# Optimization experiments

Measured on AMD Instinct MI355X. Metric: run time of the kernel, lower is better.

Reference implementation:

```python
import jax, jax.numpy as jnp
import numpy as np

NUM_CAMS, BS, NUM_QUERY, MAX_LEN, EMBED_DIMS, NPTS = 6, 1, 40000, 10000, 256, 4


def setup_inputs() -> dict:
    key = jax.random.key(0)
    kq, kr, km = jax.random.split(key, 3)
    query = jax.random.normal(kq, (BS, NUM_QUERY, EMBED_DIMS), dtype=jnp.float32)
    reference_points_cam = jax.random.normal(
        kr, (NUM_CAMS, BS, NUM_QUERY, NPTS, 2), dtype=jnp.float32)
    bev_mask = jax.random.randint(km, (NUM_CAMS, BS, NUM_QUERY, NPTS), 0, 2).astype(jnp.int32)
    return {"query": query, "reference_points_cam": reference_points_cam, "bev_mask": bev_mask}


def reference(query, reference_points_cam, bev_mask):
    # valid[c, q]: query q is seen by camera c (any of the NPTS mask bits set); bs == 1
    valid = (bev_mask > 0).any(-1)            # (cams, bs, Q) bool
    valid0 = valid[:, 0]                      # (cams, Q)

    # Stable stream compaction: valid indices first, in ascending query order.
    order = jnp.argsort(~valid0, axis=-1, stable=True)      # (cams, Q)
    indexes = order[:, :MAX_LEN].astype(jnp.int32)          # (cams, max_len)
    indexes_len = jnp.minimum(valid0.sum(-1), MAX_LEN).astype(jnp.int32)  # (cams,)

    # Padded gather/rebatch; zero out slots beyond each camera's valid count.
    pos_ok = jnp.arange(MAX_LEN)[None, :] < indexes_len[:, None]          # (cams, max_len)
    queries_rebatch = query[0][indexes]                                   # (cams, max_len, E)
    queries_rebatch = jnp.where(pos_ok[:, :, None], queries_rebatch, 0.0)

    ref0 = reference_points_cam[:, 0]                                     # (cams, Q, NPTS, 2)
    reference_points_rebatch = jax.vmap(lambda r, i: r[i])(ref0, indexes) # (cams, max_len, NPTS, 2)
    reference_points_rebatch = jnp.where(
        pos_ok[:, :, None, None], reference_points_rebatch, 0.0)

    # count_norm: 1 / (number of cameras that see each query, clamped to >= 1)
    count = valid.astype(jnp.float32).sum(0)                 # (bs, Q)
    count_norm = (1.0 / jnp.maximum(count, 1.0))[..., None]  # (bs, Q, 1)

    return (indexes,
            indexes_len,
            queries_rebatch.reshape(BS * NUM_CAMS, MAX_LEN, EMBED_DIMS),
            reference_points_rebatch.reshape(BS * NUM_CAMS, MAX_LEN, NPTS, 2),
            count_norm)
```

## Files before the change

kernel.cpp:

```cpp
#include <hip/hip_runtime.h>
#include <hip/hip_bf16.h>

#define NUM_CAMS 6
#define NQ       40000
#define MAX_LEN  10000
#define ED       256
#define NBLK     ((NQ + 255) / 256)

#define OFF_IDX  0
#define OFF_LEN  (NUM_CAMS * MAX_LEN)
#define OFF_Q    (OFF_LEN + NUM_CAMS)
#define OFF_REF  (OFF_Q + NUM_CAMS * MAX_LEN * ED)
#define OFF_CNT  (OFF_REF + NUM_CAMS * MAX_LEN * 8)

#define WS_TOT   (NUM_CAMS * NBLK)
#define WS_LEN   (WS_TOT + NUM_CAMS)

__global__ void kA_counts(const int* __restrict__ bev, float* __restrict__ out,
                          int* __restrict__ ws) {
    __shared__ int cnt[NUM_CAMS];
    const int tid = threadIdx.x;
    const int blk = blockIdx.x;
    const int q   = blk * 256 + tid;
    if (tid < NUM_CAMS) cnt[tid] = 0;
    __syncthreads();
    const int lane = tid & 63;
    const bool inb = q < NQ;
    int myCount = 0;
    for (int cam = 0; cam < NUM_CAMS; ++cam) {
        bool v = false;
        if (inb) {
            const int4 m = *reinterpret_cast<const int4*>(bev + ((size_t)cam * NQ + q) * 4);
            v = (m.x > 0) || (m.y > 0) || (m.z > 0) || (m.w > 0);
        }
        myCount += v ? 1 : 0;
        unsigned long long bal = __ballot(v);
        if (lane == 0) atomicAdd(&cnt[cam], __popcll(bal));
    }
    if (inb) out[OFF_CNT + q] = 1.0f / fmaxf((float)myCount, 1.0f);
    __syncthreads();
    if (tid < NUM_CAMS) ws[tid * NBLK + blk] = cnt[tid];
}

__global__ void kB_scan(float* __restrict__ out, int* __restrict__ ws) {
    const int cam  = blockIdx.x;
    const int lane = threadIdx.x;
    int running = 0;
    for (int base = 0; base < NBLK; base += 64) {
        const int i = base + lane;
        int val = (i < NBLK) ? ws[cam * NBLK + i] : 0;
        int v = val;
        for (int d = 1; d < 64; d <<= 1) {
            int n = __shfl_up(v, d, 64);
            if (lane >= d) v += n;
        }
        if (i < NBLK) ws[cam * NBLK + i] = v - val + running;
        running += __shfl(v, 63, 64);
    }
    if (lane == 0) {
        ws[WS_TOT + cam] = running;
        const int len = running < MAX_LEN ? running : MAX_LEN;
        ws[WS_LEN + cam] = len;
        out[OFF_LEN + cam] = (float)len;
    }
}

__global__ void kC_indexes(const int* __restrict__ bev, float* __restrict__ out,
                           const int* __restrict__ ws) {
    const int blk = blockIdx.x;
    const int cam = blockIdx.y;
    const int tid = threadIdx.x;
    const int q    = blk * 256 + tid;
    const int lane = tid & 63;
    const int wave = tid >> 6;
    const bool inb = q < NQ;
    bool v = false;
    if (inb) {
        const int4 m = *reinterpret_cast<const int4*>(bev + ((size_t)cam * NQ + q) * 4);
        v = (m.x > 0) || (m.y > 0) || (m.z > 0) || (m.w > 0);
    }
    const unsigned long long bal = __ballot(v);
    __shared__ int waveSums[4];
    if (lane == 0) waveSums[wave] = __popcll(bal);
    __syncthreads();
    int waveOff = 0;
    for (int w = 0; w < 4; ++w)
        if (w < wave) waveOff += waveSums[w];
    const int prefix   = __popcll(bal & ((1ull << lane) - 1ull));
    const int blockOff = ws[cam * NBLK + blk];
    const int total    = ws[WS_TOT + cam];
    if (inb) {
        const int vb  = blockOff + waveOff + prefix;
        const int pos = v ? vb : (total + (q - vb));
        if (pos < MAX_LEN) out[OFF_IDX + cam * MAX_LEN + pos] = (float)q;
    }
}

__global__ void kD_gather(const float* __restrict__ query, const float* __restrict__ refp,
                          float* __restrict__ out, const int* __restrict__ ws) {
    const int tid   = threadIdx.x;
    const int rowId = blockIdx.x * 4 + (tid >> 6);
    const int lane  = tid & 63;
    const int cam   = rowId / MAX_LEN;
    const int j     = rowId - cam * MAX_LEN;
    const int len   = ws[WS_LEN + cam];
    float* oq  = out + OFF_Q + (size_t)rowId * ED;
    float* orf = out + OFF_REF + (size_t)rowId * 8;
    if (j < len) {
        const int idx = (int)out[OFF_IDX + cam * MAX_LEN + j];
        const float4 v = *reinterpret_cast<const float4*>(query + (size_t)idx * ED + lane * 4);
        float2* o2 = reinterpret_cast<float2*>(oq + lane * 4);
        o2[0] = make_float2(v.x, v.y);
        o2[1] = make_float2(v.z, v.w);
        if (lane < 2) {
            const float4 r = *reinterpret_cast<const float4*>(refp + ((size_t)cam * NQ + idx) * 8 + lane * 4);
            float2* r2 = reinterpret_cast<float2*>(orf + lane * 4);
            r2[0] = make_float2(r.x, r.y);
            r2[1] = make_float2(r.z, r.w);
        }
    } else {
        float2* o2 = reinterpret_cast<float2*>(oq + lane * 4);
        o2[0] = make_float2(0.f, 0.f);
        o2[1] = make_float2(0.f, 0.f);
        if (lane < 2) {
            float2* r2 = reinterpret_cast<float2*>(orf + lane * 4);
            r2[0] = make_float2(0.f, 0.f);
            r2[1] = make_float2(0.f, 0.f);
        }
    }
}

extern "C" void kernel_launch(void* const* d_in, const int* in_sizes, int n_in,
                              void* d_out, int out_size, void* d_ws, size_t ws_size,
                              hipStream_t stream) {
    const float* query = (const float*)d_in[0];
    const float* refp  = (const float*)d_in[1];
    const int*   bev   = (const int*)d_in[2];
    float* out = (float*)d_out;
    int*   ws  = (int*)d_ws;

    kA_counts<<<NBLK, 256, 0, stream>>>(bev, out, ws);
    kB_scan<<<NUM_CAMS, 64, 0, stream>>>(out, ws);
    kC_indexes<<<dim3(NBLK, NUM_CAMS), 256, 0, stream>>>(bev, out, ws);
    kD_gather<<<(NUM_CAMS * MAX_LEN) / 4, 256, 0, stream>>>(query, refp, out, ws);
}
```

Baseline: 36.11 us.

## Replace multi-pass compaction with single-block-per-camera scan and fused gather

The count, scan and index kernels are replaced by a single kernel that uses one 1024-thread block per camera. It scans the mask chunk by chunk in order, writes compacted indices directly, and stops early once MAX_LEN valid entries are found. The count_norm computation moves into extra blocks of the gather kernel, so only two launches remain, and the gather uses nontemporal stores for the query output. The trade-off is that the scan runs serially on just six blocks with two barriers per chunk, which may be latency-bound.

```diff
diff --git a/kernel.cpp b/kernel.cpp
--- a/kernel.cpp
+++ b/kernel.cpp
@@ -5,7 +5,8 @@
 #define NQ       40000
 #define MAX_LEN  10000
 #define ED       256
-#define NBLK     ((NQ + 255) / 256)
+
+typedef float f32x2 __attribute__((ext_vector_type(2)));
 
 #define OFF_IDX  0
 #define OFF_LEN  (NUM_CAMS * MAX_LEN)
@@ -13,120 +14,130 @@
 #define OFF_REF  (OFF_Q + NUM_CAMS * MAX_LEN * ED)
 #define OFF_CNT  (OFF_REF + NUM_CAMS * MAX_LEN * 8)
 
-#define WS_TOT   (NUM_CAMS * NBLK)
-#define WS_LEN   (WS_TOT + NUM_CAMS)
+#define WS_LEN 0
 
-__global__ void kA_counts(const int* __restrict__ bev, float* __restrict__ out,
-                          int* __restrict__ ws) {
-    __shared__ int cnt[NUM_CAMS];
-    const int tid = threadIdx.x;
-    const int blk = blockIdx.x;
-    const int q   = blk * 256 + tid;
-    if (tid < NUM_CAMS) cnt[tid] = 0;
-    __syncthreads();
+#define GATHER_BLOCKS (NUM_CAMS * MAX_LEN / 4)
+#define CNT_BLOCKS    ((NQ + 255) / 256)
+
+__global__ __launch_bounds__(1024) void kScan(const int* __restrict__ bev,
+                                              float* __restrict__ out,
+                                              int* __restrict__ ws) {
+    const int cam  = blockIdx.x;
+    const int tid  = threadIdx.x;
     const int lane = tid & 63;
-    const bool inb = q < NQ;
-    int myCount = 0;
-    for (int cam = 0; cam < NUM_CAMS; ++cam) {
-        bool v = false;
-        if (inb) {
-            const int4 m = *reinterpret_cast<const int4*>(bev + ((size_t)cam * NQ + q) * 4);
-            v = (m.x > 0) || (m.y > 0) || (m.z > 0) || (m.w > 0);
+    const int wave = tid >> 6;
+    __shared__ int wsum[16];
+    const int* bevc = bev + (size_t)cam * NQ * 4;
+
+    int running = 0;
+    int4 cur = *reinterpret_cast<const int4*>(bevc + (size_t)tid * 4);
+    for (int base = 0; base < NQ; base += 1024) {
+        const int q  = base + tid;
+        const int qn = q + 1024;
+        int4 nxt = make_int4(0, 0, 0, 0);
+        if (qn < NQ) nxt = *reinterpret_cast<const int4*>(bevc + (size_t)qn * 4);
+
+        const bool v = (q < NQ) && ((cur.x > 0) | (cur.y > 0) | (cur.z > 0) | (cur.w > 0));
+        const unsigned long long bal = __ballot(v);
+        if (lane == 0) wsum[wave] = __popcll(bal);
+        __syncthreads();
+        int wOff = 0, chunkTot = 0;
+        #pragma unroll
+        for (int w = 0; w < 16; ++w) {
+            const int s = wsum[w];
+            if (w < wave) wOff += s;
+            chunkTot += s;
         }
-        myCount += v ? 1 : 0;
-        unsigned long long bal = __ballot(v);
-        if (lane == 0) atomicAdd(&cnt[cam], __popcll(bal));
+        if (v) {
+            const int pos = running + wOff + __popcll(bal & ((1ull << lane) - 1ull));
+            if (pos < MAX_LEN) out[OFF_IDX + cam * MAX_LEN + pos] = (float)q;
+        }
+        running += chunkTot;
+        __syncthreads();
+        if (running >= MAX_LEN) break;
+        cur = nxt;
     }
-    if (inb) out[OFF_CNT + q] = 1.0f / fmaxf((float)myCount, 1.0f);
-    __syncthreads();
-    if (tid < NUM_CAMS) ws[tid * NBLK + blk] = cnt[tid];
-}
+    const int total = running;
+    const int len   = total < MAX_LEN ? total : MAX_LEN;
 
-__global__ void kB_scan(float* __restrict__ out, int* __restrict__ ws) {
-    const int cam  = blockIdx.x;
-    const int lane = threadIdx.x;
-    int running = 0;
-    for (int base = 0; base < NBLK; base += 64) {
-        const int i = base + lane;
-        int val = (i < NBLK) ? ws[cam * NBLK + i] : 0;
-        int v = val;
-        for (int d = 1; d < 64; d <<= 1) {
-            int n = __shfl_up(v, d, 64);
-            if (lane >= d) v += n;
+    if (total < MAX_LEN) {
+        int runInv = 0;
+        for (int base = 0; base < NQ; base += 1024) {
+            const int q = base + tid;
+            bool v = false;
+            if (q < NQ) {
+                const int4 m = *reinterpret_cast<const int4*>(bevc + (size_t)q * 4);
+                v = (m.x > 0) | (m.y > 0) | (m.z > 0) | (m.w > 0);
+            }
+            const bool inv = (q < NQ) && !v;
+            const unsigned long long bal = __ballot(inv);
+            if (lane == 0) wsum[wave] = __popcll(bal);
+            __syncthreads();
+            int wOff = 0, chunkTot = 0;
+            #pragma unroll
+            for (int w = 0; w < 16; ++w) {
+                const int s = wsum[w];
+                if (w < wave) wOff += s;
+                chunkTot += s;
+            }
+            if (inv) {
+                const int pos = total + runInv + wOff + __popcll(bal & ((1ull << lane) - 1ull));
+                if (pos < MAX_LEN) out[OFF_IDX + cam * MAX_LEN + pos] = (float)q;
+            }
+            runInv += chunkTot;
+            __syncthreads();
+            if (total + runInv >= MAX_LEN) break;
         }
-        if (i < NBLK) ws[cam * NBLK + i] = v - val + running;
-        running += __shfl(v, 63, 64);
     }
-    if (lane == 0) {
-        ws[WS_TOT + cam] = running;
-        const int len = running < MAX_LEN ? running : MAX_LEN;
+    if (tid == 0) {
         ws[WS_LEN + cam] = len;
         out[OFF_LEN + cam] = (float)len;
     }
 }
 
-__global__ void kC_indexes(const int* __restrict__ bev, float* __restrict__ out,
-                           const int* __restrict__ ws) {
+__global__ void kGather(const float* __restrict__ query, const float* __restrict__ refp,
+                        float* __restrict__ out, const int* __restrict__ ws,
+                        const int* __restrict__ bev) {
     const int blk = blockIdx.x;
-    const int cam = blockIdx.y;
     const int tid = threadIdx.x;
-    const int q    = blk * 256 + tid;
-    const int lane = tid & 63;
-    const int wave = tid >> 6;
-    const bool inb = q < NQ;
-    bool v = false;
-    if (inb) {
-        const int4 m = *reinterpret_cast<const int4*>(bev + ((size_t)cam * NQ + q) * 4);
-        v = (m.x > 0) || (m.y > 0) || (m.z > 0) || (m.w > 0);
+    if (blk >= GATHER_BLOCKS) {
+        const int q = (blk - GATHER_BLOCKS) * 256 + tid;
+        if (q < NQ) {
+            int cnt = 0;
+            #pragma unroll
+            for (int cam = 0; cam < NUM_CAMS; ++cam) {
+                const int4 m = *reinterpret_cast<const int4*>(bev + ((size_t)cam * NQ + q) * 4);
+                cnt += ((m.x > 0) | (m.y > 0) | (m.z > 0) | (m.w > 0)) ? 1 : 0;
+            }
+            out[OFF_CNT + q] = 1.0f / fmaxf((float)cnt, 1.0f);
+        }
+        return;
     }
-    const unsigned long long bal = __ballot(v);
-    __shared__ int waveSums[4];
-    if (lane == 0) waveSums[wave] = __popcll(bal);
-    __syncthreads();
-    int waveOff = 0;
-    for (int w = 0; w < 4; ++w)
-        if (w < wave) waveOff += waveSums[w];
-    const int prefix   = __popcll(bal & ((1ull << lane) - 1ull));
-    const int blockOff = ws[cam * NBLK + blk];
-    const int total    = ws[WS_TOT + cam];
-    if (inb) {
-        const int vb  = blockOff + waveOff + prefix;
-        const int pos = v ? vb : (total + (q - vb));
-        if (pos < MAX_LEN) out[OFF_IDX + cam * MAX_LEN + pos] = (float)q;
-    }
-}
-
-__global__ void kD_gather(const float* __restrict__ query, const float* __restrict__ refp,
-                          float* __restrict__ out, const int* __restrict__ ws) {
-    const int tid   = threadIdx.x;
-    const int rowId = blockIdx.x * 4 + (tid >> 6);
+    const int rowId = blk * 4 + (tid >> 6);
     const int lane  = tid & 63;
     const int cam   = rowId / MAX_LEN;
     const int j     = rowId - cam * MAX_LEN;
     const int len   = ws[WS_LEN + cam];
-    float* oq  = out + OFF_Q + (size_t)rowId * ED;
-    float* orf = out + OFF_REF + (size_t)rowId * 8;
+
+    f32x2 a = (f32x2)(0.f), b = (f32x2)(0.f), r0 = (f32x2)(0.f), r1 = (f32x2)(0.f);
     if (j < len) {
         const int idx = (int)out[OFF_IDX + cam * MAX_LEN + j];
-        const float4 v = *reinterpret_cast<const float4*>(query + (size_t)idx * ED + lane * 4);
-        float2* o2 = reinterpret_cast<float2*>(oq + lane * 4);
-        o2[0] = make_float2(v.x, v.y);
-        o2[1] = make_float2(v.z, v.w);
+        const float4 vq = *reinterpret_cast<const float4*>(query + (size_t)idx * ED + lane * 4);
+        a.x = vq.x; a.y = vq.y;
+        b.x = vq.z; b.y = vq.w;
         if (lane < 2) {
             const float4 r = *reinterpret_cast<const float4*>(refp + ((size_t)cam * NQ + idx) * 8 + lane * 4);
-            float2* r2 = reinterpret_cast<float2*>(orf + lane * 4);
-            r2[0] = make_float2(r.x, r.y);
-            r2[1] = make_float2(r.z, r.w);
+            r0.x = r.x; r0.y = r.y;
+            r1.x = r.z; r1.y = r.w;
         }
-    } else {
-        float2* o2 = reinterpret_cast<float2*>(oq + lane * 4);
-        o2[0] = make_float2(0.f, 0.f);
-        o2[1] = make_float2(0.f, 0.f);
-        if (lane < 2) {
-            float2* r2 = reinterpret_cast<float2*>(orf + lane * 4);
-            r2[0] = make_float2(0.f, 0.f);
-            r2[1] = make_float2(0.f, 0.f);
-        }
+    }
+    f32x2* o2 = reinterpret_cast<f32x2*>(out + OFF_Q + (size_t)rowId * ED + lane * 4);
+    __builtin_nontemporal_store(a, o2);
+    __builtin_nontemporal_store(b, o2 + 1);
+    if (lane < 2) {
+        f32x2* r2 = reinterpret_cast<f32x2*>(out + OFF_REF + (size_t)rowId * 8 + lane * 4);
+        r2[0] = r0;
+        r2[1] = r1;
     }
 }
 
@@ -139,8 +150,6 @@
     float* out = (float*)d_out;
     int*   ws  = (int*)d_ws;
 
-    kA_counts<<<NBLK, 256, 0, stream>>>(bev, out, ws);
-    kB_scan<<<NUM_CAMS, 64, 0, stream>>>(out, ws);
-    kC_indexes<<<dim3(NBLK, NUM_CAMS), 256, 0, stream>>>(bev, out, ws);
-    kD_gather<<<(NUM_CAMS * MAX_LEN) / 4, 256, 0, stream>>>(query, refp, out, ws);
+    kScan<<<NUM_CAMS, 1024, 0, stream>>>(bev, out, ws);
+    kGather<<<GATHER_BLOCKS + CNT_BLOCKS, 256, 0, stream>>>(query, refp, out, ws, bev);
 }
```

Measured after the change: 36.79 us. About the same (+1.9%).

## Scatter queries by source with per-camera position map to reuse query loads

Applied to the files above, without the earlier changes.

kC_indexes now also writes a per-camera, per-query destination position into the workspace whenever the workspace is large enough. A new source-ordered gather kernel then loads each query row once and scatters it to every camera slot that sees it, using nontemporal stores. Separate blocks zero the padded tail rows. This removes the repeated reads of the same query row from different cameras, at the cost of an extra position array write and read, and less regular store addresses. A fallback kernel keeps the old destination-ordered gather and also recomputes count_norm.

```diff
diff --git a/kernel.cpp b/kernel.cpp
--- a/kernel.cpp
+++ b/kernel.cpp
@@ -7,14 +7,24 @@
 #define ED       256
 #define NBLK     ((NQ + 255) / 256)
 
+typedef float f32x2 __attribute__((ext_vector_type(2)));
+
 #define OFF_IDX  0
 #define OFF_LEN  (NUM_CAMS * MAX_LEN)
 #define OFF_Q    (OFF_LEN + NUM_CAMS)
 #define OFF_REF  (OFF_Q + NUM_CAMS * MAX_LEN * ED)
 #define OFF_CNT  (OFF_REF + NUM_CAMS * MAX_LEN * 8)
 
-#define WS_TOT   (NUM_CAMS * NBLK)
-#define WS_LEN   (WS_TOT + NUM_CAMS)
+#define WS_OFF 0
+#define WS_TOT (NUM_CAMS * NBLK)
+#define WS_LEN (WS_TOT + NUM_CAMS)
+#define WS_POS (WS_LEN + NUM_CAMS + 6)
+#define WS_NEED_BYTES ((WS_POS + NUM_CAMS * NQ) * 4)
+
+#define QBLOCKS      (NQ / 4)
+#define TAIL_BLOCKS  (NUM_CAMS * MAX_LEN / 4)
+#define CNT_BLOCKS   ((NQ + 255) / 256)
+#define GATHER_BLOCKS (NUM_CAMS * MAX_LEN / 4)
 
 __global__ void kA_counts(const int* __restrict__ bev, float* __restrict__ out,
                           int* __restrict__ ws) {
@@ -27,11 +37,12 @@
     const int lane = tid & 63;
     const bool inb = q < NQ;
     int myCount = 0;
+    #pragma unroll
     for (int cam = 0; cam < NUM_CAMS; ++cam) {
         bool v = false;
         if (inb) {
             const int4 m = *reinterpret_cast<const int4*>(bev + ((size_t)cam * NQ + q) * 4);
-            v = (m.x > 0) || (m.y > 0) || (m.z > 0) || (m.w > 0);
+            v = (m.x > 0) | (m.y > 0) | (m.z > 0) | (m.w > 0);
         }
         myCount += v ? 1 : 0;
         unsigned long long bal = __ballot(v);
@@ -39,7 +50,7 @@
     }
     if (inb) out[OFF_CNT + q] = 1.0f / fmaxf((float)myCount, 1.0f);
     __syncthreads();
-    if (tid < NUM_CAMS) ws[tid * NBLK + blk] = cnt[tid];
+    if (tid < NUM_CAMS) ws[WS_OFF + tid * NBLK + blk] = cnt[tid];
 }
 
 __global__ void kB_scan(float* __restrict__ out, int* __restrict__ ws) {
@@ -48,13 +59,13 @@
     int running = 0;
     for (int base = 0; base < NBLK; base += 64) {
         const int i = base + lane;
-        int val = (i < NBLK) ? ws[cam * NBLK + i] : 0;
+        int val = (i < NBLK) ? ws[WS_OFF + cam * NBLK + i] : 0;
         int v = val;
         for (int d = 1; d < 64; d <<= 1) {
             int n = __shfl_up(v, d, 64);
             if (lane >= d) v += n;
         }
-        if (i < NBLK) ws[cam * NBLK + i] = v - val + running;
+        if (i < NBLK) ws[WS_OFF + cam * NBLK + i] = v - val + running;
         running += __shfl(v, 63, 64);
     }
     if (lane == 0) {
@@ -66,7 +77,7 @@
 }
 
 __global__ void kC_indexes(const int* __restrict__ bev, float* __restrict__ out,
-                           const int* __restrict__ ws) {
+                           int* __restrict__ ws, int usePos) {
     const int blk = blockIdx.x;
     const int cam = blockIdx.y;
     const int tid = threadIdx.x;
@@ -77,56 +88,119 @@
     bool v = false;
     if (inb) {
         const int4 m = *reinterpret_cast<const int4*>(bev + ((size_t)cam * NQ + q) * 4);
-        v = (m.x > 0) || (m.y > 0) || (m.z > 0) || (m.w > 0);
+        v = (m.x > 0) | (m.y > 0) | (m.z > 0) | (m.w > 0);
     }
     const unsigned long long bal = __ballot(v);
     __shared__ int waveSums[4];
     if (lane == 0) waveSums[wave] = __popcll(bal);
     __syncthreads();
     int waveOff = 0;
+    #pragma unroll
     for (int w = 0; w < 4; ++w)
         if (w < wave) waveOff += waveSums[w];
     const int prefix   = __popcll(bal & ((1ull << lane) - 1ull));
-    const int blockOff = ws[cam * NBLK + blk];
+    const int blockOff = ws[WS_OFF + cam * NBLK + blk];
     const int total    = ws[WS_TOT + cam];
     if (inb) {
         const int vb  = blockOff + waveOff + prefix;
         const int pos = v ? vb : (total + (q - vb));
         if (pos < MAX_LEN) out[OFF_IDX + cam * MAX_LEN + pos] = (float)q;
-    }
-}
-
-__global__ void kD_gather(const float* __restrict__ query, const float* __restrict__ refp,
-                          float* __restrict__ out, const int* __restrict__ ws) {
+        if (usePos) ws[WS_POS + cam * NQ + q] = (v && vb < MAX_LEN) ? vb : -1;
+    }
+}
+
+__global__ void kGatherQ(const float* __restrict__ query, const float* __restrict__ refp,
+                         float* __restrict__ out, const int* __restrict__ ws) {
+    const int blk   = blockIdx.x;
     const int tid   = threadIdx.x;
-    const int rowId = blockIdx.x * 4 + (tid >> 6);
+    const int group = tid >> 6;
+    const int lane  = tid & 63;
+    if (blk >= QBLOCKS) {
+        const int rowId = (blk - QBLOCKS) * 4 + group;
+        const int cam   = rowId / MAX_LEN;
+        const int j     = rowId - cam * MAX_LEN;
+        if (j < ws[WS_LEN + cam]) return;
+        const f32x2 z = (f32x2)(0.f);
+        f32x2* o2 = reinterpret_cast<f32x2*>(out + OFF_Q + (size_t)rowId * ED + lane * 4);
+        o2[0] = z; o2[1] = z;
+        if (lane < 4)
+            *reinterpret_cast<f32x2*>(out + OFF_REF + (size_t)rowId * 8 + lane * 2) = z;
+        return;
+    }
+    const int q = blk * 4 + group;
+
+    int pos[NUM_CAMS];
+    bool any = false;
+    #pragma unroll
+    for (int cam = 0; cam < NUM_CAMS; ++cam) {
+        const int p = ws[WS_POS + cam * NQ + q];
+        pos[cam] = p;
+        any |= (p >= 0);
+    }
+    if (!any) return;
+
+    const float4 vq = *reinterpret_cast<const float4*>(query + (size_t)q * ED + lane * 4);
+    f32x2 a; a.x = vq.x; a.y = vq.y;
+    f32x2 b; b.x = vq.z; b.y = vq.w;
+
+    #pragma unroll
+    for (int cam = 0; cam < NUM_CAMS; ++cam) {
+        const int p = pos[cam];
+        if (p >= 0) {
+            f32x2* o2 = reinterpret_cast<f32x2*>(out + OFF_Q + ((size_t)cam * MAX_LEN + p) * ED + lane * 4);
+            __builtin_nontemporal_store(a, o2);
+            __builtin_nontemporal_store(b, o2 + 1);
+            if (lane < 4) {
+                const f32x2 r = *reinterpret_cast<const f32x2*>(refp + ((size_t)cam * NQ + q) * 8 + lane * 2);
+                *reinterpret_cast<f32x2*>(out + OFF_REF + ((size_t)cam * MAX_LEN + p) * 8 + lane * 2) = r;
+            }
+        }
+    }
+}
+
+__global__ void kGather(const float* __restrict__ query, const float* __restrict__ refp,
+                        float* __restrict__ out, const int* __restrict__ ws,
+                        const int* __restrict__ bev) {
+    const int blk = blockIdx.x;
+    const int tid = threadIdx.x;
+    if (blk >= GATHER_BLOCKS) {
+        const int q = (blk - GATHER_BLOCKS) * 256 + tid;
+        if (q < NQ) {
+            int cnt = 0;
+            #pragma unroll
+            for (int cam = 0; cam < NUM_CAMS; ++cam) {
+                const int4 m = *reinterpret_cast<const int4*>(bev + ((size_t)cam * NQ + q) * 4);
+                cnt += ((m.x > 0) | (m.y > 0) | (m.z > 0) | (m.w > 0)) ? 1 : 0;
+            }
+            out[OFF_CNT + q] = 1.0f / fmaxf((float)cnt, 1.0f);
+        }
+        return;
+    }
+    const int rowId = blk * 4 + (tid >> 6);
     const int lane  = tid & 63;
     const int cam   = rowId / MAX_LEN;
     const int j     = rowId - cam * MAX_LEN;
     const int len   = ws[WS_LEN + cam];
-    float* oq  = out + OFF_Q + (size_t)rowId * ED;
-    float* orf = out + OFF_REF + (size_t)rowId * 8;
+
+    f32x2 a = (f32x2)(0.f), b = (f32x2)(0.f), r0 = (f32x2)(0.f), r1 = (f32x2)(0.f);
     if (j < len) {
         const int idx = (int)out[OFF_IDX + cam * MAX_LEN + j];
-        const float4 v = *reinterpret_cast<const float4*>(query + (size_t)idx * ED + lane * 4);
-        float2* o2 = reinterpret_cast<float2*>(oq + lane * 4);
-        o2[0] = make_float2(v.x, v.y);
-        o2[1] = make_float2(v.z, v.w);
+        const float4 vq = *reinterpret_cast<const float4*>(query + (size_t)idx * ED + lane * 4);
+        a.x = vq.x; a.y = vq.y;
+        b.x = vq.z; b.y = vq.w;
         if (lane < 2) {
             const float4 r = *reinterpret_cast<const float4*>(refp + ((size_t)cam * NQ + idx) * 8 + lane * 4);
-            float2* r2 = reinterpret_cast<float2*>(orf + lane * 4);
-            r2[0] = make_float2(r.x, r.y);
-            r2[1] = make_float2(r.z, r.w);
-        }
-    } else {
-        float2* o2 = reinterpret_cast<float2*>(oq + lane * 4);
-        o2[0] = make_float2(0.f, 0.f);
-        o2[1] = make_float2(0.f, 0.f);
-        if (lane < 2) {
-            float2* r2 = reinterpret_cast<float2*>(orf + lane * 4);
-            r2[0] = make_float2(0.f, 0.f);
-            r2[1] = make_float2(0.f, 0.f);
-        }
+            r0.x = r.x; r0.y = r.y;
+            r1.x = r.z; r1.y = r.w;
+        }
+    }
+    f32x2* o2 = reinterpret_cast<f32x2*>(out + OFF_Q + (size_t)rowId * ED + lane * 4);
+    __builtin_nontemporal_store(a, o2);
+    __builtin_nontemporal_store(b, o2 + 1);
+    if (lane < 2) {
+        f32x2* r2 = reinterpret_cast<f32x2*>(out + OFF_REF + (size_t)rowId * 8 + lane * 4);
+        r2[0] = r0;
+        r2[1] = r1;
     }
 }
 
@@ -138,9 +212,14 @@
     const int*   bev   = (const int*)d_in[2];
     float* out = (float*)d_out;
     int*   ws  = (int*)d_ws;
+    const int usePos = (ws_size >= (size_t)WS_NEED_BYTES) ? 1 : 0;
 
     kA_counts<<<NBLK, 256, 0, stream>>>(bev, out, ws);
     kB_scan<<<NUM_CAMS, 64, 0, stream>>>(out, ws);
-    kC_indexes<<<dim3(NBLK, NUM_CAMS), 256, 0, stream>>>(bev, out, ws);
-    kD_gather<<<(NUM_CAMS * MAX_LEN) / 4, 256, 0, stream>>>(query, refp, out, ws);
-}
+    kC_indexes<<<dim3(NBLK, NUM_CAMS), 256, 0, stream>>>(bev, out, ws, usePos);
+    if (usePos) {
+        kGatherQ<<<QBLOCKS + TAIL_BLOCKS, 256, 0, stream>>>(query, refp, out, ws);
+    } else {
+        kGather<<<GATHER_BLOCKS + CNT_BLOCKS, 256, 0, stream>>>(query, refp, out, ws, bev);
+    }
+}
```

Result: faster. 34.51 us (-4.5%).
